# Kernel optimization log

Hardware: AMD Instinct MI355X
Metric: run time of the kernel (lower is better)

## Reference

```python
import jax, jax.numpy as jnp
import numpy as np

TEMPERATURE = 1.0


def setup_inputs() -> dict:
    key = jax.random.key(0)
    kq, kk, kv = jax.random.split(key, 3)
    shape = (2, 16, 2048, 64)  # B, H, L, D
    q = jax.random.normal(kq, shape, dtype=jnp.float32)
    k = jax.random.normal(kk, shape, dtype=jnp.float32)
    v = jax.random.normal(kv, shape, dtype=jnp.float32)
    return {"q": q, "k": k, "v": v}


def reference(q, k, v):
    # q, k, v: [B, H, L, D]
    L = q.shape[2]
    # scores: [B, H, L, L]; note: divided by temperature, NOT sqrt(D), per source
    scores = jnp.einsum("bhqd,bhkd->bhqk", q, k) / TEMPERATURE
    # causal mask: position j > i masked with -inf
    causal = jnp.tril(jnp.ones((L, L), dtype=bool))  # True = keep
    scores = jnp.where(causal, scores, -jnp.inf)
    attn = jax.nn.softmax(scores, axis=-1)
    out = jnp.einsum("bhqk,bhkd->bhqd", attn, v)
    return out
```

## Files before the change

kernel.cpp:

```cpp
#include <hip/hip_runtime.h>
#include <math.h>


typedef __attribute__((ext_vector_type(8))) _Float16 f16x8;
typedef __attribute__((ext_vector_type(4))) _Float16 f16x4;
typedef __attribute__((ext_vector_type(2))) _Float16 f16x2;
typedef __attribute__((ext_vector_type(4))) float f32x4;
typedef __attribute__((ext_vector_type(16))) float f32x16;
typedef unsigned short u16;
typedef unsigned int u32;
typedef __attribute__((ext_vector_type(8))) u16 u16x8;
typedef __attribute__((ext_vector_type(4))) u32 u32x4;

constexpr int Lq = 2048;
constexpr int Dd = 64;
constexpr int KT = 64;
constexpr int BH = 32;

#define SWZB(row, bcol) ((((row) * 128) + (bcol)) ^ (((row) & 7) << 4))

#define GLOAD_LDS16(g, l)                                                     \
  __builtin_amdgcn_global_load_lds(                                           \
      (const __attribute__((address_space(1))) void*)(g),                     \
      (__attribute__((address_space(3))) void*)(l), 16, 0, 0)

static __device__ __forceinline__ u16 f2h(float x) {
  return __builtin_bit_cast(u16, (_Float16)x);
}

constexpr int PREP_KB = (BH * Lq * Dd) / (256 * 16);

__global__ __launch_bounds__(256)
void attn_prep(const float* __restrict__ K, const float* __restrict__ V,
               u16* __restrict__ Kh, u16* __restrict__ VTh) {
  const int b = blockIdx.x;
  const int tid = threadIdx.x;
  if (b < PREP_KB) {
    const size_t base = ((size_t)b * 256 + tid) * 16;
    const f32x4* src = reinterpret_cast<const f32x4*>(K + base);
    u16x8 o0, o1;
    #pragma unroll
    for (int i = 0; i < 2; ++i) {
      const f32x4 a = src[i];
      #pragma unroll
      for (int j = 0; j < 4; ++j) o0[i * 4 + j] = f2h(a[j]);
    }
    #pragma unroll
    for (int i = 0; i < 2; ++i) {
      const f32x4 a = src[2 + i];
      #pragma unroll
      for (int j = 0; j < 4; ++j) o1[i * 4 + j] = f2h(a[j]);
    }
    *reinterpret_cast<u16x8*>(Kh + base) = o0;
    *reinterpret_cast<u16x8*>(Kh + base + 8) = o1;
  } else {
    __shared__ u16 lt[64][66];
    const int vb = b - PREP_KB;
    const int h = vb >> 5, tt = vb & 31;
    const float* Vt = V + ((size_t)h * Lq + tt * 64) * Dd;
    const int r = tid & 63, dg = tid >> 6;
    #pragma unroll
    for (int i = 0; i < 4; ++i) {
      const f32x4 a = *reinterpret_cast<const f32x4*>(Vt + (size_t)r * Dd + dg * 16 + i * 4);
      #pragma unroll
      for (int j = 0; j < 2; ++j) {
        const unsigned two =
            (unsigned)f2h(a[2 * j]) | ((unsigned)f2h(a[2 * j + 1]) << 16);
        *reinterpret_cast<unsigned*>(&lt[r][dg * 16 + i * 4 + j * 2]) = two;
      }
    }
    __syncthreads();
    const int d = tid >> 2, kq = tid & 3;
    u16x8 w0, w1;
    #pragma unroll
    for (int j = 0; j < 8; ++j) w0[j] = lt[kq * 16 + j][d];
    #pragma unroll
    for (int j = 0; j < 8; ++j) w1[j] = lt[kq * 16 + 8 + j][d];
    u16* dst = VTh + ((size_t)h * Dd + d) * Lq + tt * 64 + kq * 16;
    *reinterpret_cast<u16x8*>(dst) = w0;
    *reinterpret_cast<u16x8*>(dst + 8) = w1;
  }
}

__global__ __launch_bounds__(128)
void attn_main(const float* __restrict__ Q, float* __restrict__ O,
               const u16* __restrict__ Kh, const u16* __restrict__ VTh) {
  __shared__ char ks[2][8192];
  __shared__ char vt2[2][8192];
  __shared__ float bc[2][32];

  const int tid  = threadIdx.x;
  const int lane = tid & 63;
  const int wv   = tid >> 6;
  const int l31  = lane & 31;
  const int hi   = lane >> 5;

  const int b = blockIdx.x;
  const int j = b >> 8;
  const int i = b & 255;
  const int h = i >> 3;
  const int p = i & 7;
  const int chunk = (j == 0) ? p : (j == 1) ? (31 - p) : (j == 2) ? (p + 8) : (23 - p);

  const float* Qb = Q + (size_t)h * Lq * Dd;
  float*       Ob = O + (size_t)h * Lq * Dd;
  const u16*   Kb = Kh + (size_t)h * Lq * Dd;
  const u16*   Vb = VTh + (size_t)h * Dd * Lq;

  const int row0 = chunk * 64;
  const int T    = chunk + 1;
  const int qrow = row0 + wv * 32;

  f16x8 qf[4];
  #pragma unroll
  for (int kc = 0; kc < 4; ++kc) {
    const float* qp = Qb + (size_t)(qrow + l31) * Dd + kc * 16 + hi * 8;
    const f32x4 a = *reinterpret_cast<const f32x4*>(qp);
    const f32x4 c = *reinterpret_cast<const f32x4*>(qp + 4);
    f16x8 q8;
    #pragma unroll
    for (int e = 0; e < 4; ++e) {
      q8[e]     = (_Float16)a[e];
      q8[e + 4] = (_Float16)c[e];
    }
    qf[kc] = q8;
  }

  float m = -INFINITY, lsum = 0.f;
  f32x16 o0, o1;
  #pragma unroll
  for (int e = 0; e < 16; ++e) { o0[e] = 0.f; o1[e] = 0.f; }

  const int rr = lane >> 3;
  const int c0 = (lane & 7) ^ rr;

  #pragma unroll
  for (int it = 0; it < 4; ++it) {
    const int row = wv * 32 + it * 8 + rr;
    GLOAD_LDS16(Kb + (size_t)row * Dd + c0 * 8,
                &ks[0][wv * 4096 + it * 1024 + lane * 16]);
    GLOAD_LDS16(Vb + (size_t)row * Lq + c0 * 8,
                &vt2[0][wv * 4096 + it * 1024 + lane * 16]);
  }

  int cur = 0;
  #pragma unroll 1
  for (int t = 0; t < T; ++t) {
    __syncthreads();
    if (t + 1 < T) {
      #pragma unroll
      for (int it = 0; it < 4; ++it) {
        const int row = wv * 32 + it * 8 + rr;
        GLOAD_LDS16(Kb + (size_t)((t + 1) * KT + row) * Dd + c0 * 8,
                    &ks[cur ^ 1][wv * 4096 + it * 1024 + lane * 16]);
        GLOAD_LDS16(Vb + (size_t)row * Lq + (t + 1) * KT + c0 * 8,
                    &vt2[cur ^ 1][wv * 4096 + it * 1024 + lane * 16]);
      }
    }
    const char* kb = ks[cur];
    const char* vb = vt2[cur];
    const bool last  = (t == T - 1);
    const bool have1 = !(last && wv == 0);

    f32x16 st0, st1;
    #pragma unroll
    for (int e = 0; e < 16; ++e) { st0[e] = 0.f; st1[e] = 0.f; }
    __builtin_amdgcn_s_setprio(1);
    #pragma unroll
    for (int kc = 0; kc < 4; ++kc) {
      const f16x8 kf = *reinterpret_cast<const f16x8*>(
          kb + SWZB(l31, kc * 32 + hi * 16));
      st0 = __builtin_amdgcn_mfma_f32_32x32x16_f16(kf, qf[kc], st0, 0, 0, 0);
    }
    if (have1) {
      #pragma unroll
      for (int kc = 0; kc < 4; ++kc) {
        const f16x8 kf = *reinterpret_cast<const f16x8*>(
            kb + SWZB(32 + l31, kc * 32 + hi * 16));
        st1 = __builtin_amdgcn_mfma_f32_32x32x16_f16(kf, qf[kc], st1, 0, 0, 0);
      }
    }
    __builtin_amdgcn_s_setprio(0);

    if (last) {
      #pragma unroll
      for (int r = 0; r < 16; ++r) {
        const int crow = (r & 3) + 8 * (r >> 2) + 4 * hi;
        if (wv == 0) { if (crow > l31) st0[r] = -INFINITY; }
        else         { if (crow > l31) st1[r] = -INFINITY; }
      }
    }

    float pm = st0[0];
    #pragma unroll
    for (int r = 1; r < 16; ++r) pm = fmaxf(pm, st0[r]);
    if (have1) {
      #pragma unroll
      for (int r = 0; r < 16; ++r) pm = fmaxf(pm, st1[r]);
    }
    pm = fmaxf(pm, __shfl_xor(pm, 32));

    if (__any(pm > m + 8.f)) {
      const float mn = fmaxf(m, pm);
      const float sc = __expf(m - mn);
      m = mn;
      lsum *= sc;
      if (hi == 0) bc[wv][l31] = sc;
      const f32x4 s0 = *reinterpret_cast<const f32x4*>(&bc[wv][4 * hi]);
      const f32x4 s1 = *reinterpret_cast<const f32x4*>(&bc[wv][8 + 4 * hi]);
      const f32x4 s2 = *reinterpret_cast<const f32x4*>(&bc[wv][16 + 4 * hi]);
      const f32x4 s3 = *reinterpret_cast<const f32x4*>(&bc[wv][24 + 4 * hi]);
      #pragma unroll
      for (int r = 0; r < 16; ++r) {
        const float fac = (r < 4) ? s0[r & 3] : (r < 8) ? s1[r & 3]
                        : (r < 12) ? s2[r & 3] : s3[r & 3];
        o0[r] *= fac;
        o1[r] *= fac;
      }
    }

    float rs = 0.f;
    #pragma unroll
    for (int r = 0; r < 16; ++r) { st0[r] = __expf(st0[r] - m); rs += st0[r]; }
    if (have1) {
      #pragma unroll
      for (int r = 0; r < 16; ++r) { st1[r] = __expf(st1[r] - m); rs += st1[r]; }
    }
    rs += __shfl_xor(rs, 32);
    lsum += rs;

    #pragma unroll
    for (int ksub = 0; ksub < 2; ++ksub) {
      if (ksub == 1 && !have1) break;
      const f32x16& st = (ksub == 0) ? st0 : st1;
      #pragma unroll
      for (int ks2 = 0; ks2 < 2; ++ks2) {
        const u32 pe0 = __builtin_bit_cast(u32,
            __builtin_amdgcn_cvt_pkrtz(st[8 * ks2 + 0], st[8 * ks2 + 1]));
        const u32 pe1 = __builtin_bit_cast(u32,
            __builtin_amdgcn_cvt_pkrtz(st[8 * ks2 + 2], st[8 * ks2 + 3]));
        const u32 po0 = __builtin_bit_cast(u32,
            __builtin_amdgcn_cvt_pkrtz(st[8 * ks2 + 4], st[8 * ks2 + 5]));
        const u32 po1 = __builtin_bit_cast(u32,
            __builtin_amdgcn_cvt_pkrtz(st[8 * ks2 + 6], st[8 * ks2 + 7]));
        const u32 re0 = __shfl_xor(pe0, 32);
        const u32 re1 = __shfl_xor(pe1, 32);
        const u32 ro0 = __shfl_xor(po0, 32);
        const u32 ro1 = __shfl_xor(po1, 32);
        u32x4 w;
        w[0] = hi ? ro0 : pe0;
        w[1] = hi ? ro1 : pe1;
        w[2] = hi ? po0 : re0;
        w[3] = hi ? po1 : re1;
        const f16x8 pa = __builtin_bit_cast(f16x8, w);
        const int cb = ksub * 64 + ks2 * 32 + hi * 16;
        const f16x8 v0 = *reinterpret_cast<const f16x8*>(vb + SWZB(l31, cb));
        const f16x8 v1 = *reinterpret_cast<const f16x8*>(vb + SWZB(32 + l31, cb));
        __builtin_amdgcn_s_setprio(1);
        o0 = __builtin_amdgcn_mfma_f32_32x32x16_f16(pa, v0, o0, 0, 0, 0);
        o1 = __builtin_amdgcn_mfma_f32_32x32x16_f16(pa, v1, o1, 0, 0, 0);
        __builtin_amdgcn_s_setprio(0);
      }
    }
    cur ^= 1;
  }

  const float inv = 1.f / lsum;
  if (hi == 0) bc[wv][l31] = inv;
  const f32x4 i0 = *reinterpret_cast<const f32x4*>(&bc[wv][4 * hi]);
  const f32x4 i1 = *reinterpret_cast<const f32x4*>(&bc[wv][8 + 4 * hi]);
  const f32x4 i2 = *reinterpret_cast<const f32x4*>(&bc[wv][16 + 4 * hi]);
  const f32x4 i3 = *reinterpret_cast<const f32x4*>(&bc[wv][24 + 4 * hi]);
  #pragma unroll
  for (int r = 0; r < 16; ++r) {
    const int crow = (r & 3) + 8 * (r >> 2) + 4 * hi;
    const float fac = (r < 4) ? i0[r & 3] : (r < 8) ? i1[r & 3]
                    : (r < 12) ? i2[r & 3] : i3[r & 3];
    float* op = Ob + (size_t)(qrow + crow) * Dd + l31;
    op[0]  = o0[r] * fac;
    op[32] = o1[r] * fac;
  }
}

__global__ __launch_bounds__(256)
void causal_attn_fb(const float* __restrict__ Q, const float* __restrict__ K,
                    const float* __restrict__ V, float* __restrict__ O) {
  __shared__ char ks[2][KT * 128];
  __shared__ char vt[2][Dd * 128];
  __shared__ char pl[4][16 * 128];
  const int tid = threadIdx.x, lane = tid & 63, wv = tid >> 6;
  const int l15 = lane & 15, g = lane >> 4;
  const int kg = tid & 15, dq = tid >> 4;
  const int bh = blockIdx.x / 16, pr = blockIdx.x % 16;
  const size_t base = (size_t)bh * Lq * Dd;
  const float* Qb = Q + base; const float* Kb = K + base;
  const float* Vb = V + base; float* Ob = O + base;
  char* pw = pl[wv];
  #pragma unroll 1
  for (int phase = 0; phase < 2; ++phase) {
    const int chunk = (phase == 0) ? pr : (31 - pr);
    const int row0 = chunk * 64, T = chunk + 1, qrow = row0 + wv * 16;
    f16x8 qf[2];
    #pragma unroll
    for (int kk = 0; kk < 2; ++kk) {
      const float* qp = Qb + (size_t)(qrow + l15) * Dd + kk * 32 + g * 8;
      const f32x4 a = *reinterpret_cast<const f32x4*>(qp);
      const f32x4 b = *reinterpret_cast<const f32x4*>(qp + 4);
      f16x8 q8;
      #pragma unroll
      for (int i = 0; i < 4; ++i) { q8[i] = (_Float16)a[i]; q8[i+4] = (_Float16)b[i]; }
      qf[kk] = q8;
    }
    float m[4], lsum[4]; f32x4 o[4];
    #pragma unroll
    for (int r = 0; r < 4; ++r) { m[r] = -INFINITY; lsum[r] = 0.f; }
    #pragma unroll
    for (int nd = 0; nd < 4; ++nd) o[nd] = f32x4{0.f, 0.f, 0.f, 0.f};
    {
      f32x4 kreg[4], vreg[4];
      #pragma unroll
      for (int i = 0; i < 4; ++i) {
        const int c = tid + i * 256;
        kreg[i] = *reinterpret_cast<const f32x4*>(Kb + (size_t)(c >> 4) * Dd + (c & 15) * 4);
      }
      #pragma unroll
      for (int c = 0; c < 4; ++c)
        vreg[c] = *reinterpret_cast<const f32x4*>(Vb + (size_t)(kg * 4 + c) * Dd + dq * 4);
      __syncthreads();
      #pragma unroll
      for (int i = 0; i < 4; ++i) {
        const int c = tid + i * 256;
        f16x4 hh;
        #pragma unroll
        for (int jj = 0; jj < 4; ++jj) hh[jj] = (_Float16)kreg[i][jj];
        *reinterpret_cast<f16x4*>(ks[0] + SWZB(c >> 4, (c & 15) * 8)) = hh;
      }
      #pragma unroll
      for (int jj = 0; jj < 4; ++jj) {
        f16x4 hh;
        #pragma unroll
        for (int c = 0; c < 4; ++c) hh[c] = (_Float16)vreg[c][jj];
        *reinterpret_cast<f16x4*>(vt[0] + SWZB(dq * 4 + jj, kg * 8)) = hh;
      }
    }
    int cur = 0;
    #pragma unroll 1
    for (int t = 0; t < T; ++t) {
      __syncthreads();
      const char* kb = ks[cur]; const char* vb = vt[cur];
      f32x4 kreg[4], vreg[4];
      const bool pfn = (t + 1 < T);
      if (pfn) {
        const float* Kt = Kb + (size_t)(t + 1) * KT * Dd;
        const float* Vt = Vb + (size_t)(t + 1) * KT * Dd;
        #pragma unroll
        for (int i = 0; i < 4; ++i) {
          const int c = tid + i * 256;
          kreg[i] = *reinterpret_cast<const f32x4*>(Kt + (size_t)(c >> 4) * Dd + (c & 15) * 4);
        }
        #pragma unroll
        for (int c = 0; c < 4; ++c)
          vreg[c] = *reinterpret_cast<const f32x4*>(Vt + (size_t)(kg * 4 + c) * Dd + dq * 4);
      }
      f32x4 s[4];
      #pragma unroll
      for (int n = 0; n < 4; ++n) s[n] = f32x4{0.f, 0.f, 0.f, 0.f};
      #pragma unroll
      for (int kk = 0; kk < 2; ++kk) {
        #pragma unroll
        for (int n = 0; n < 4; ++n) {
          const f16x8 kf = *reinterpret_cast<const f16x8*>(kb + SWZB(n * 16 + l15, kk * 64 + g * 16));
          s[n] = __builtin_amdgcn_mfma_f32_16x16x32_f16(qf[kk], kf, s[n], 0, 0, 0);
        }
      }
      if (t == T - 1) {
        #pragma unroll
        for (int n = 0; n < 4; ++n) {
          const int key = t * KT + n * 16 + l15;
          #pragma unroll
          for (int r = 0; r < 4; ++r)
            if (key > qrow + 4 * g + r) s[n][r] = -INFINITY;
        }
      }
      float rmax[4], rsum[4], scale[4];
      #pragma unroll
      for (int r = 0; r < 4; ++r)
        rmax[r] = fmaxf(fmaxf(s[0][r], s[1][r]), fmaxf(s[2][r], s[3][r]));
      #pragma unroll
      for (int mk = 1; mk <= 8; mk <<= 1) {
        #pragma unroll
        for (int r = 0; r < 4; ++r) rmax[r] = fmaxf(rmax[r], __shfl_xor(rmax[r], mk));
      }
      #pragma unroll
      for (int r = 0; r < 4; ++r) {
        const float mn = fmaxf(m[r], rmax[r]);
        scale[r] = __expf(m[r] - mn); m[r] = mn;
      }
      #pragma unroll
      for (int n = 0; n < 4; ++n) {
        #pragma unroll
        for (int r = 0; r < 4; ++r) s[n][r] = __expf(s[n][r] - m[r]);
      }
      #pragma unroll
      for (int r = 0; r < 4; ++r) rsum[r] = (s[0][r] + s[1][r]) + (s[2][r] + s[3][r]);
      #pragma unroll
      for (int mk = 1; mk <= 8; mk <<= 1) {
        #pragma unroll
        for (int r = 0; r < 4; ++r) rsum[r] += __shfl_xor(rsum[r], mk);
      }
      #pragma unroll
      for (int r = 0; r < 4; ++r) lsum[r] = lsum[r] * scale[r] + rsum[r];
      #pragma unroll
      for (int nd = 0; nd < 4; ++nd) {
        #pragma unroll
        for (int r = 0; r < 4; ++r) o[nd][r] *= scale[r];
      }
      #pragma unroll
      for (int n = 0; n < 4; ++n) {
        #pragma unroll
        for (int r = 0; r < 4; ++r)
          *reinterpret_cast<_Float16*>(pw + SWZB(4 * g + r, (n * 16 + l15) * 2)) = (_Float16)s[n][r];
      }
      asm volatile("s_waitcnt lgkmcnt(0)" ::: "memory");
      __builtin_amdgcn_sched_barrier(0);
      #pragma unroll
      for (int kblk = 0; kblk < 2; ++kblk) {
        const f16x8 pf = *reinterpret_cast<const f16x8*>(pw + SWZB(l15, kblk * 64 + g * 16));
        #pragma unroll
        for (int nd = 0; nd < 4; ++nd) {
          const f16x8 vf = *reinterpret_cast<const f16x8*>(vb + SWZB(nd * 16 + l15, kblk * 64 + g * 16));
          o[nd] = __builtin_amdgcn_mfma_f32_16x16x32_f16(pf, vf, o[nd], 0, 0, 0);
        }
      }
      if (pfn) {
        char* kn = ks[cur ^ 1]; char* vn = vt[cur ^ 1];
        #pragma unroll
        for (int i = 0; i < 4; ++i) {
          const int c = tid + i * 256;
          f16x4 hh;
          #pragma unroll
          for (int jj = 0; jj < 4; ++jj) hh[jj] = (_Float16)kreg[i][jj];
          *reinterpret_cast<f16x4*>(kn + SWZB(c >> 4, (c & 15) * 8)) = hh;
        }
        #pragma unroll
        for (int jj = 0; jj < 4; ++jj) {
          f16x4 hh;
          #pragma unroll
          for (int c = 0; c < 4; ++c) hh[c] = (_Float16)vreg[c][jj];
          *reinterpret_cast<f16x4*>(vn + SWZB(dq * 4 + jj, kg * 8)) = hh;
        }
      }
      cur ^= 1;
    }
    float inv[4];
    #pragma unroll
    for (int r = 0; r < 4; ++r) inv[r] = 1.f / lsum[r];
    #pragma unroll
    for (int nd = 0; nd < 4; ++nd) {
      #pragma unroll
      for (int r = 0; r < 4; ++r)
        Ob[(size_t)(qrow + 4 * g + r) * Dd + nd * 16 + l15] = o[nd][r] * inv[r];
    }
  }
}

extern "C" void kernel_launch(void* const* d_in, const int* in_sizes, int n_in,
                              void* d_out, int out_size, void* d_ws, size_t ws_size,
                              hipStream_t stream) {
  const float* q = (const float*)d_in[0];
  const float* k = (const float*)d_in[1];
  const float* v = (const float*)d_in[2];
  float* o = (float*)d_out;
  const size_t elems = (size_t)BH * Lq * Dd;
  const size_t need = elems * 2 * 2;
  if (ws_size >= need) {
    u16* Kh = (u16*)d_ws;
    u16* VTh = Kh + elems;
    attn_prep<<<dim3(2 * PREP_KB), dim3(256), 0, stream>>>(k, v, Kh, VTh);
    attn_main<<<dim3(BH * 32), dim3(128), 0, stream>>>(q, o, Kh, VTh);
  } else {
    causal_attn_fb<<<dim3(BH * 16), dim3(256), 0, stream>>>(q, k, v, o);
  }
  (void)in_sizes; (void)n_in; (void)out_size;
}
```

Baseline: 78.71 us.

## Fold log2e into Q, use exp2, tree reductions, halve shuffles, reorder block schedule

Q is pre-scaled by log2(e) when converted to fp16, so softmax exponentials become exp2 with no per-element multiply. Max and sum reductions become balanced trees to shorten dependency chains. The P-fragment exchange now uses two cross-half shuffles per step instead of four by selecting which value each half sends. Block-to-chunk mapping changes to a simple heaviest-chunk-first order across heads, replacing the interleaved balancing pattern. Scaling Q before the fp16 rounding slightly changes numerics.

```diff
diff --git a/kernel.cpp b/kernel.cpp
--- a/kernel.cpp
+++ b/kernel.cpp
@@ -4,7 +4,6 @@
 
 typedef __attribute__((ext_vector_type(8))) _Float16 f16x8;
 typedef __attribute__((ext_vector_type(4))) _Float16 f16x4;
-typedef __attribute__((ext_vector_type(2))) _Float16 f16x2;
 typedef __attribute__((ext_vector_type(4))) float f32x4;
 typedef __attribute__((ext_vector_type(16))) float f32x16;
 typedef unsigned short u16;
@@ -16,6 +15,7 @@
 constexpr int Dd = 64;
 constexpr int KT = 64;
 constexpr int BH = 32;
+constexpr float LOG2E = 1.44269504088896f;
 
 #define SWZB(row, bcol) ((((row) * 128) + (bcol)) ^ (((row) & 7) << 4))
 
@@ -26,6 +26,21 @@
 
 static __device__ __forceinline__ u16 f2h(float x) {
   return __builtin_bit_cast(u16, (_Float16)x);
+}
+
+static __device__ __forceinline__ float tmax16(const f32x16& v) {
+  float a = fmaxf(v[0], v[1]), b = fmaxf(v[2], v[3]);
+  float c = fmaxf(v[4], v[5]), d = fmaxf(v[6], v[7]);
+  float e = fmaxf(v[8], v[9]), f = fmaxf(v[10], v[11]);
+  float g = fmaxf(v[12], v[13]), h = fmaxf(v[14], v[15]);
+  a = fmaxf(a, b); c = fmaxf(c, d); e = fmaxf(e, f); g = fmaxf(g, h);
+  return fmaxf(fmaxf(a, c), fmaxf(e, g));
+}
+static __device__ __forceinline__ float tsum16(const f32x16& v) {
+  float a = v[0] + v[1], b = v[2] + v[3], c = v[4] + v[5], d = v[6] + v[7];
+  float e = v[8] + v[9], f = v[10] + v[11], g = v[12] + v[13], h = v[14] + v[15];
+  a += b; c += d; e += f; g += h;
+  return (a + c) + (e + g);
 }
 
 constexpr int PREP_KB = (BH * Lq * Dd) / (256 * 16);
@@ -96,20 +111,16 @@
   const int hi   = lane >> 5;
 
   const int b = blockIdx.x;
-  const int j = b >> 8;
-  const int i = b & 255;
-  const int h = i >> 3;
-  const int p = i & 7;
-  const int chunk = (j == 0) ? p : (j == 1) ? (31 - p) : (j == 2) ? (p + 8) : (23 - p);
+  const int chunk = 31 - (b >> 5);
+  const int h = b & 31;
 
   const float* Qb = Q + (size_t)h * Lq * Dd;
   float*       Ob = O + (size_t)h * Lq * Dd;
   const u16*   Kb = Kh + (size_t)h * Lq * Dd;
   const u16*   Vb = VTh + (size_t)h * Dd * Lq;
 
-  const int row0 = chunk * 64;
   const int T    = chunk + 1;
-  const int qrow = row0 + wv * 32;
+  const int qrow = chunk * 64 + wv * 32;
 
   f16x8 qf[4];
   #pragma unroll
@@ -120,8 +131,8 @@
     f16x8 q8;
     #pragma unroll
     for (int e = 0; e < 4; ++e) {
-      q8[e]     = (_Float16)a[e];
-      q8[e + 4] = (_Float16)c[e];
+      q8[e]     = (_Float16)(a[e] * LOG2E);
+      q8[e + 4] = (_Float16)(c[e] * LOG2E);
     }
     qf[kc] = q8;
   }
@@ -191,18 +202,13 @@
       }
     }
 
-    float pm = st0[0];
-    #pragma unroll
-    for (int r = 1; r < 16; ++r) pm = fmaxf(pm, st0[r]);
-    if (have1) {
-      #pragma unroll
-      for (int r = 0; r < 16; ++r) pm = fmaxf(pm, st1[r]);
-    }
+    float pm = tmax16(st0);
+    if (have1) pm = fmaxf(pm, tmax16(st1));
     pm = fmaxf(pm, __shfl_xor(pm, 32));
 
-    if (__any(pm > m + 8.f)) {
+    if (__any(pm > m + 8.f * LOG2E)) {
       const float mn = fmaxf(m, pm);
-      const float sc = __expf(m - mn);
+      const float sc = exp2f(m - mn);
       m = mn;
       lsum *= sc;
       if (hi == 0) bc[wv][l31] = sc;
@@ -219,12 +225,13 @@
       }
     }
 
-    float rs = 0.f;
-    #pragma unroll
-    for (int r = 0; r < 16; ++r) { st0[r] = __expf(st0[r] - m); rs += st0[r]; }
+    #pragma unroll
+    for (int r = 0; r < 16; ++r) st0[r] = exp2f(st0[r] - m);
+    float rs = tsum16(st0);
     if (have1) {
       #pragma unroll
-      for (int r = 0; r < 16; ++r) { st1[r] = __expf(st1[r] - m); rs += st1[r]; }
+      for (int r = 0; r < 16; ++r) st1[r] = exp2f(st1[r] - m);
+      rs += tsum16(st1);
     }
     rs += __shfl_xor(rs, 32);
     lsum += rs;
@@ -243,15 +250,13 @@
             __builtin_amdgcn_cvt_pkrtz(st[8 * ks2 + 4], st[8 * ks2 + 5]));
         const u32 po1 = __builtin_bit_cast(u32,
             __builtin_amdgcn_cvt_pkrtz(st[8 * ks2 + 6], st[8 * ks2 + 7]));
-        const u32 re0 = __shfl_xor(pe0, 32);
-        const u32 re1 = __shfl_xor(pe1, 32);
-        const u32 ro0 = __shfl_xor(po0, 32);
-        const u32 ro1 = __shfl_xor(po1, 32);
+        const u32 ss0 = __shfl_xor(hi ? pe0 : po0, 32);
+        const u32 ss1 = __shfl_xor(hi ? pe1 : po1, 32);
         u32x4 w;
-        w[0] = hi ? ro0 : pe0;
-        w[1] = hi ? ro1 : pe1;
-        w[2] = hi ? po0 : re0;
-        w[3] = hi ? po1 : re1;
+        w[0] = hi ? ss0 : pe0;
+        w[1] = hi ? ss1 : pe1;
+        w[2] = hi ? po0 : ss0;
+        w[3] = hi ? po1 : ss1;
         const f16x8 pa = __builtin_bit_cast(f16x8, w);
         const int cb = ksub * 64 + ks2 * 32 + hi * 16;
         const f16x8 v0 = *reinterpret_cast<const f16x8*>(vb + SWZB(l31, cb));
```

Result: slower. 84.43 us (+7.3%).
